# Optimization experiments

Measured on AMD Instinct MI355X. Metric: run time of the kernel, lower is better.

## Reference

```python
import jax, jax.numpy as jnp
import numpy as np

D_EMB = 1024
B, T = 8, 2048

def setup_inputs() -> dict:
    key = jax.random.key(0)
    ks = jax.random.split(key, 7)
    s = 0.02
    return {
        "x": jax.random.normal(ks[0], (B, T, D_EMB), dtype=jnp.float32),
        "W_attn": jax.random.normal(ks[1], (3 * D_EMB, D_EMB), dtype=jnp.float32) * s,
        "b_attn": jax.random.normal(ks[2], (3 * D_EMB,), dtype=jnp.float32) * s,
        "W_proj": jax.random.normal(ks[3], (D_EMB, D_EMB), dtype=jnp.float32) * s,
        "b_proj": jax.random.normal(ks[4], (D_EMB,), dtype=jnp.float32) * s,
        "W_fc": jax.random.normal(ks[5], (1, D_EMB), dtype=jnp.float32) * s,
        "b_fc": jax.random.normal(ks[6], (1,), dtype=jnp.float32) * s,
    }

def reference(x, W_attn, b_attn, W_proj, b_proj, W_fc, b_fc):
    # qkv projection: torch Linear => x @ W.T + b
    qkv = jnp.einsum('btc,dc->btd', x, W_attn) + b_attn          # [B,T,3C]
    q, k, v = jnp.split(qkv, 3, axis=2)                          # each [B,T,C]
    scale = q.shape[-1] ** (-0.5)
    attn_scores = jnp.einsum('btc,bsc->bts', q, k) * scale       # [B,T,T]
    attn_weights = jax.nn.softmax(attn_scores, axis=-1)          # traditional softmax
    y = jnp.einsum('bts,bsc->btc', attn_weights, v)              # [B,T,C]
    y = jnp.einsum('btc,dc->btd', y, W_proj) + b_proj            # [B,T,C]
    out = jnp.einsum('btc,oc->bto', y, W_fc) + b_fc              # [B,T,1]
    return out
```

## Files before the change

### kernel.cpp

```cpp
#include <hip/hip_runtime.h>
#include <stdint.h>

#define D_EMB 1024
#define NBATCH 8
#define SEQ 2048
#define MTOT (NBATCH*SEQ)

typedef __attribute__((ext_vector_type(8))) short short8;
typedef __attribute__((ext_vector_type(4))) float f32x4;

__device__ __forceinline__ ushort bf16r(float x) {
  union { float f; uint32_t u; } c; c.f = x;
  return (ushort)((c.u + 0x7fffu + ((c.u >> 16) & 1u)) >> 16);
}

__device__ __forceinline__ void cp16(const ushort* g, ushort* l) {
  __builtin_amdgcn_global_load_lds(
      (const __attribute__((address_space(1))) void*)g,
      (__attribute__((address_space(3))) void*)l, 16, 0, 0);
}

__global__ __launch_bounds__(256) void cvt_w(
    const float4* __restrict__ Wattn4, const float* __restrict__ bproj,
    const float* __restrict__ Wfc, const float* __restrict__ bfc,
    ushort* __restrict__ wt, float* __restrict__ w_eff, float* __restrict__ wv_eff,
    float* __restrict__ v_eff, float4* __restrict__ numden4, float* __restrict__ sc) {
  int tid = threadIdx.x;
  int b = blockIdx.x;
  __shared__ ushort lt[64][68];
  __shared__ float red[4];
  if (b < 512) {
    int td = b & 31, tc = b >> 5;
    #pragma unroll
    for (int rep = 0; rep < 4; rep++) {
      int i = (tid >> 4) + rep * 16;
      int jj = tid & 15;
      float4 v = Wattn4[(long)(td * 64 + i) * 256 + tc * 16 + jj];
      lt[i][jj * 4 + 0] = bf16r(v.x);
      lt[i][jj * 4 + 1] = bf16r(v.y);
      lt[i][jj * 4 + 2] = bf16r(v.z);
      lt[i][jj * 4 + 3] = bf16r(v.w);
    }
    __syncthreads();
    #pragma unroll
    for (int rep = 0; rep < 2; rep++) {
      int c = (tid >> 3) + rep * 32;
      int d0 = (tid & 7) * 8;
      short8 o;
      #pragma unroll
      for (int k = 0; k < 8; k++) o[k] = (short)lt[d0 + k][c];
      *(short8*)(wt + (long)(tc * 64 + c) * 2048 + td * 64 + d0) = o;
    }
    return;
  }
  int b2 = b - 512;
  if (b2 == 0) {
    for (int i = tid; i < 1024; i += 256) { w_eff[i] = 0.f; wv_eff[i] = 0.f; v_eff[i] = 0.f; }
    return;
  }
  if (b2 == 1) {
    float v = 0.f;
    #pragma unroll
    for (int i = 0; i < 4; i++) { int c = tid + i * 256; v += bproj[c] * Wfc[c]; }
    int lane = tid & 63, w = tid >> 6;
    #pragma unroll
    for (int off = 32; off; off >>= 1) v += __shfl_xor(v, off);
    if (lane == 0) red[w] = v;
    __syncthreads();
    if (tid == 0) sc[0] = red[0] + red[1] + red[2] + red[3] + bfc[0];
    return;
  }
  numden4[(long)(b2 - 2) * 256 + tid] = make_float4(0.f, 0.f, 0.f, 0.f);
}

__global__ void prep1(const float* __restrict__ Wp, const float* __restrict__ Wfc,
                      const float* __restrict__ Wattn, const float* __restrict__ battn,
                      float* __restrict__ w_eff, float* __restrict__ v_eff) {
  int c = blockIdx.x * 256 + threadIdx.x;
  if (blockIdx.y < 64) {
    int d0 = blockIdx.y * 16;
    float s = 0.f;
    #pragma unroll
    for (int d = d0; d < d0 + 16; d++) s += Wfc[d] * Wp[(long)d * D_EMB + c];
    atomicAdd(&w_eff[c], s);
  } else {
    int d0 = (blockIdx.y - 64) * 16;
    float s = 0.f;
    #pragma unroll
    for (int d = d0; d < d0 + 16; d++) s += battn[d] * Wattn[(long)(1024 + d) * D_EMB + c];
    atomicAdd(&v_eff[c], s);
  }
}

__global__ void prep2(const float* __restrict__ Wattn, const float* __restrict__ battn,
                      const float* __restrict__ w_eff, float* __restrict__ wv_eff,
                      float* __restrict__ sc) {
  int tid = threadIdx.x;
  if (blockIdx.y == 64) {
    if (blockIdx.x != 0) return;
    float v = 0.f;
    #pragma unroll
    for (int i = 0; i < 4; i++) { int c = tid + i * 256; v += battn[2048 + c] * w_eff[c]; }
    int lane = tid & 63, w = tid >> 6;
    #pragma unroll
    for (int off = 32; off; off >>= 1) v += __shfl_xor(v, off);
    __shared__ float red[4];
    if (lane == 0) red[w] = v;
    __syncthreads();
    if (tid == 0) sc[1] = red[0] + red[1] + red[2] + red[3];
    return;
  }
  int d = blockIdx.x * 256 + tid;
  int c0 = blockIdx.y * 16;
  float s = 0.f;
  #pragma unroll
  for (int c = c0; c < c0 + 16; c++) s += w_eff[c] * Wattn[(long)(2048 + c) * D_EMB + d];
  atomicAdd(&wv_eff[d], s);
}

template<int MODE>
__device__ __forceinline__ void gemm_body(
    int bx, int by, int z, ushort* lds_a, ushort* lds_b,
    const ushort* __restrict__ A, long lda, long sAz,
    const ushort* __restrict__ B, long ldb, long sBz,
    ushort* __restrict__ C, long ldc, float scale, int K,
    const float* __restrict__ vw, const float* __restrict__ bb,
    float* __restrict__ num, float* __restrict__ den) {
  const ushort* Az = A + (long)z * sAz;
  const ushort* Bz = B + (long)z * sBz;
  long m0 = (long)by * 128, n0 = (long)bx * 128;
  int t = threadIdx.x;
  int wave = t >> 6, lane = t & 63;
  int r = lane & 15, q = lane >> 4;
  int wm = (wave & 1) * 64, wn = (wave >> 1) * 64;

  f32x4 acc[4][4] = {};

  int row0 = t >> 3;
  int kc = (t & 7) ^ (row0 & 7);
  const ushort* Ap = Az + (m0 + row0) * lda + kc * 8;
  const ushort* Bp = Bz + (n0 + row0) * ldb + kc * 8;
  long a32 = 32 * lda, b32 = 32 * ldb;

  int swz = r & 7;

  #pragma unroll 1
  for (int k0 = 0; k0 < K; k0 += 64) {
    if (k0) __syncthreads();
    cp16(Ap + k0,            lds_a + t * 8);
    cp16(Ap + k0 + a32,      lds_a + (t + 256) * 8);
    cp16(Ap + k0 + 2 * a32,  lds_a + (t + 512) * 8);
    cp16(Ap + k0 + 3 * a32,  lds_a + (t + 768) * 8);
    cp16(Bp + k0,            lds_b + t * 8);
    cp16(Bp + k0 + b32,      lds_b + (t + 256) * 8);
    cp16(Bp + k0 + 2 * b32,  lds_b + (t + 512) * 8);
    cp16(Bp + k0 + 3 * b32,  lds_b + (t + 768) * 8);
    __syncthreads();
    #pragma unroll
    for (int kk = 0; kk < 2; kk++) {
      int cidx = (kk * 4 + q) ^ swz;
      short8 af[4], bf[4];
      #pragma unroll
      for (int i = 0; i < 4; i++)
        af[i] = *(const short8*)(lds_a + ((wm + i * 16 + r) * 8 + cidx) * 8);
      #pragma unroll
      for (int j = 0; j < 4; j++)
        bf[j] = *(const short8*)(lds_b + ((wn + j * 16 + r) * 8 + cidx) * 8);
      #pragma unroll
      for (int i = 0; i < 4; i++)
        #pragma unroll
        for (int j = 0; j < 4; j++)
          acc[i][j] = __builtin_amdgcn_mfma_f32_16x16x32_bf16(af[i], bf[j], acc[i][j], 0, 0, 0);
    }
  }

  if (MODE == 0) {
    #pragma unroll
    for (int i = 0; i < 4; i++) {
      #pragma unroll
      for (int j = 0; j < 4; j++) {
        long col = n0 + wn + j * 16 + r;
        #pragma unroll
        for (int rr = 0; rr < 4; rr++) {
          long row = m0 + wm + i * 16 + q * 4 + rr;
          C[row * ldc + col] = bf16r(acc[i][j][rr] * scale);
        }
      }
    }
  } else {
    const float* vwz = vw + (long)z * SEQ + n0;
    const float* bbz = bb + (long)z * SEQ + n0;
    float* numz = num + (long)z * SEQ + m0;
    float* denz = den + (long)z * SEQ + m0;
    float vwj[4], bbj[4];
    #pragma unroll
    for (int j = 0; j < 4; j++) {
      vwj[j] = vwz[wn + j * 16 + r];
      bbj[j] = bbz[wn + j * 16 + r];
    }
    #pragma unroll
    for (int i = 0; i < 4; i++) {
      #pragma unroll
      for (int rr = 0; rr < 4; rr++) {
        float sn = 0.f, sd = 0.f;
        #pragma unroll
        for (int j = 0; j < 4; j++) {
          float e = __expf((acc[i][j][rr] + bbj[j]) * scale);
          sd += e;
          sn += e * vwj[j];
        }
        #pragma unroll
        for (int off = 1; off < 16; off <<= 1) {
          sn += __shfl_xor(sn, off);
          sd += __shfl_xor(sd, off);
        }
        if (r == 0) {
          int row = wm + i * 16 + q * 4 + rr;
          atomicAdd(&numz[row], sn);
          atomicAdd(&denz[row], sd);
        }
      }
    }
  }
}

__global__ __launch_bounds__(256, 4) void cvt_mt(
    const float4* __restrict__ x4, const float4* __restrict__ wv4,
    const float4* __restrict__ v4, const float* __restrict__ sc,
    ushort* __restrict__ xb, float* __restrict__ vw, float* __restrict__ bb,
    const ushort* __restrict__ wt, ushort* __restrict__ mt) {
  __shared__ __align__(16) ushort lds_a[128 * 64];
  __shared__ __align__(16) ushort lds_b[128 * 64];
  int tid = threadIdx.x;
  if (blockIdx.x < 64) {
    int b = blockIdx.x;
    gemm_body<0>(b & 7, b >> 3, 0, lds_a, lds_b,
                 wt + 1024, 2048L, 0L, wt, 2048L, 0L,
                 mt, 1024L, 1.0f, D_EMB, nullptr, nullptr, nullptr, nullptr);
    return;
  }
  int wave = tid >> 6, lane = tid & 63;
  long row = (long)(blockIdx.x - 64) * 4 + wave;
  const float4* xr = x4 + row * 256;
  ushort* xo = xb + row * D_EMB;
  float s = 0.f, s2 = 0.f;
  #pragma unroll
  for (int i = 0; i < 4; i++) {
    int idx = lane + i * 64;
    float4 v = xr[idx];
    float4 w = wv4[idx];
    float4 u = v4[idx];
    *(ushort4*)(xo + idx * 4) = make_ushort4(bf16r(v.x), bf16r(v.y), bf16r(v.z), bf16r(v.w));
    s  += v.x * w.x + v.y * w.y + v.z * w.z + v.w * w.w;
    s2 += v.x * u.x + v.y * u.y + v.z * u.z + v.w * u.w;
  }
  #pragma unroll
  for (int off = 32; off; off >>= 1) { s += __shfl_xor(s, off); s2 += __shfl_xor(s2, off); }
  if (lane == 0) { vw[row] = s + sc[1]; bb[row] = s2; }
}

template<int MODE, int RMODE>
__global__ __launch_bounds__(256, 4) void gemm_nt(
    const ushort* __restrict__ A, long lda, long sAz,
    const ushort* __restrict__ B, long ldb, long sBz,
    ushort* __restrict__ C, long ldc, float scale, int K,
    const float* __restrict__ vw, const float* __restrict__ bb,
    float* __restrict__ num, float* __restrict__ den) {
  __shared__ __align__(16) ushort lds_a[128 * 64];
  __shared__ __align__(16) ushort lds_b[128 * 64];
  int bx, by, z;
  if (RMODE == 1) {
    int f = (int)(blockIdx.x + 8u * blockIdx.y);
    int xcd = f & 7, g = f >> 3;
    by = xcd * 16 + (g & 15); bx = g >> 4; z = 0;
  } else {
    bx = blockIdx.x; by = blockIdx.y; z = blockIdx.z;
  }
  gemm_body<MODE>(bx, by, z, lds_a, lds_b, A, lda, sAz, B, ldb, sBz,
                  C, ldc, scale, K, vw, bb, num, den);
}

__global__ __launch_bounds__(256) void finalize(
    const float* __restrict__ num, const float* __restrict__ den,
    const float* __restrict__ sc, float* __restrict__ out) {
  long i = blockIdx.x * 256L + threadIdx.x;
  out[i] = num[i] / den[i] + sc[0];
}

extern "C" void kernel_launch(void* const* d_in, const int* in_sizes, int n_in,
                              void* d_out, int out_size, void* d_ws, size_t ws_size,
                              hipStream_t stream) {
  const float* x     = (const float*)d_in[0];
  const float* Wattn = (const float*)d_in[1];
  const float* battn = (const float*)d_in[2];
  const float* Wproj = (const float*)d_in[3];
  const float* bproj = (const float*)d_in[4];
  const float* Wfc   = (const float*)d_in[5];
  const float* bfc   = (const float*)d_in[6];
  float* out = (float*)d_out;

  const size_t OFF_XB    = 0;
  const size_t OFF_WT    = 33554432;
  const size_t OFF_MT    = 37748736;
  const size_t OFF_XM    = 39845888;
  const size_t OFF_NUM   = 73400320;
  const size_t OFF_DEN   = 73465856;
  const size_t OFF_VW    = 73531392;
  const size_t OFF_BB    = 73596928;
  const size_t OFF_WEFF  = 73662464;
  const size_t OFF_WVEFF = 73666560;
  const size_t OFF_VEFF  = 73670656;
  const size_t OFF_SC    = 73674752;
  const size_t NEED      = 73674760;
  if (ws_size < NEED) return;

  char* ws = (char*)d_ws;
  ushort* xb    = (ushort*)(ws + OFF_XB);
  ushort* wt    = (ushort*)(ws + OFF_WT);
  ushort* mt    = (ushort*)(ws + OFF_MT);
  ushort* xm    = (ushort*)(ws + OFF_XM);
  float* num    = (float*)(ws + OFF_NUM);
  float* den    = (float*)(ws + OFF_DEN);
  float* vw     = (float*)(ws + OFF_VW);
  float* bb     = (float*)(ws + OFF_BB);
  float* w_eff  = (float*)(ws + OFF_WEFF);
  float* wv_eff = (float*)(ws + OFF_WVEFF);
  float* v_eff  = (float*)(ws + OFF_VEFF);
  float* sc     = (float*)(ws + OFF_SC);

  cvt_w<<<dim3(546), dim3(256), 0, stream>>>(
      (const float4*)Wattn, bproj, Wfc, bfc, wt, w_eff, wv_eff, v_eff, (float4*)num, sc);

  prep1<<<dim3(4, 128), dim3(256), 0, stream>>>(Wproj, Wfc, Wattn, battn, w_eff, v_eff);

  prep2<<<dim3(4, 65), dim3(256), 0, stream>>>(Wattn, battn, w_eff, wv_eff, sc);

  cvt_mt<<<dim3(64 + 4096), dim3(256), 0, stream>>>(
      (const float4*)x, (const float4*)wv_eff, (const float4*)v_eff, sc, xb, vw, bb, wt, mt);

  gemm_nt<0, 1><<<dim3(8, 128, 1), dim3(256), 0, stream>>>(
      xb, (long)D_EMB, 0L, mt, (long)D_EMB, 0L,
      xm, (long)D_EMB, 1.0f, D_EMB, nullptr, nullptr, nullptr, nullptr);

  gemm_nt<1, 0><<<dim3(16, 16, NBATCH), dim3(256), 0, stream>>>(
      xm, (long)D_EMB, (long)SEQ * D_EMB, xb, (long)D_EMB, (long)SEQ * D_EMB,
      nullptr, 0L, 0.03125f, D_EMB, vw, bb, num, den);

  finalize<<<dim3(64), dim3(256), 0, stream>>>(num, den, sc, out);
}
```

Measured before the change: 260.8 us.

## Split-K the Wq·Wk product and fold it into the prep kernels

The 1024x1024 Wq^T·Wk weight product was computed by only 64 blocks with the full K=1024, sharing a launch with the x conversion. It is now split into 8 K-slices of 128. That gives 512 GEMM blocks, which run alongside the prep1 reductions in one launch and write fp32 partials. A new prep2red kernel sums the partials and converts them to bf16, and the x conversion becomes its own kernel. Launch bounds on the GEMM are raised to 5 waves per SIMD. The split adds an fp32 partial buffer round trip through memory in exchange for much more parallelism on the tail-bound weight GEMM.

Result: slower. 555.1 us (+112.9%).

```diff
diff --git a/kernel.cpp b/kernel.cpp
--- a/kernel.cpp
+++ b/kernel.cpp
@@ -73,57 +73,12 @@
   numden4[(long)(b2 - 2) * 256 + tid] = make_float4(0.f, 0.f, 0.f, 0.f);
 }
 
-__global__ void prep1(const float* __restrict__ Wp, const float* __restrict__ Wfc,
-                      const float* __restrict__ Wattn, const float* __restrict__ battn,
-                      float* __restrict__ w_eff, float* __restrict__ v_eff) {
-  int c = blockIdx.x * 256 + threadIdx.x;
-  if (blockIdx.y < 64) {
-    int d0 = blockIdx.y * 16;
-    float s = 0.f;
-    #pragma unroll
-    for (int d = d0; d < d0 + 16; d++) s += Wfc[d] * Wp[(long)d * D_EMB + c];
-    atomicAdd(&w_eff[c], s);
-  } else {
-    int d0 = (blockIdx.y - 64) * 16;
-    float s = 0.f;
-    #pragma unroll
-    for (int d = d0; d < d0 + 16; d++) s += battn[d] * Wattn[(long)(1024 + d) * D_EMB + c];
-    atomicAdd(&v_eff[c], s);
-  }
-}
-
-__global__ void prep2(const float* __restrict__ Wattn, const float* __restrict__ battn,
-                      const float* __restrict__ w_eff, float* __restrict__ wv_eff,
-                      float* __restrict__ sc) {
-  int tid = threadIdx.x;
-  if (blockIdx.y == 64) {
-    if (blockIdx.x != 0) return;
-    float v = 0.f;
-    #pragma unroll
-    for (int i = 0; i < 4; i++) { int c = tid + i * 256; v += battn[2048 + c] * w_eff[c]; }
-    int lane = tid & 63, w = tid >> 6;
-    #pragma unroll
-    for (int off = 32; off; off >>= 1) v += __shfl_xor(v, off);
-    __shared__ float red[4];
-    if (lane == 0) red[w] = v;
-    __syncthreads();
-    if (tid == 0) sc[1] = red[0] + red[1] + red[2] + red[3];
-    return;
-  }
-  int d = blockIdx.x * 256 + tid;
-  int c0 = blockIdx.y * 16;
-  float s = 0.f;
-  #pragma unroll
-  for (int c = c0; c < c0 + 16; c++) s += w_eff[c] * Wattn[(long)(2048 + c) * D_EMB + d];
-  atomicAdd(&wv_eff[d], s);
-}
-
 template<int MODE>
 __device__ __forceinline__ void gemm_body(
     int bx, int by, int z, ushort* lds_a, ushort* lds_b,
     const ushort* __restrict__ A, long lda, long sAz,
     const ushort* __restrict__ B, long ldb, long sBz,
-    ushort* __restrict__ C, long ldc, float scale, int K,
+    ushort* __restrict__ C, long ldc, float* __restrict__ fC, float scale, int K,
     const float* __restrict__ vw, const float* __restrict__ bb,
     float* __restrict__ num, float* __restrict__ den) {
   const ushort* Az = A + (long)z * sAz;
@@ -187,6 +142,20 @@
         }
       }
     }
+  } else if (MODE == 2) {
+    float* fz = fC + (long)z * 1048576;
+    #pragma unroll
+    for (int i = 0; i < 4; i++) {
+      #pragma unroll
+      for (int j = 0; j < 4; j++) {
+        long col = n0 + wn + j * 16 + r;
+        #pragma unroll
+        for (int rr = 0; rr < 4; rr++) {
+          long row = m0 + wm + i * 16 + q * 4 + rr;
+          fz[row * 1024 + col] = acc[i][j][rr];
+        }
+      }
+    }
   } else {
     const float* vwz = vw + (long)z * SEQ + n0;
     const float* bbz = bb + (long)z * SEQ + n0;
@@ -224,23 +193,89 @@
   }
 }
 
-__global__ __launch_bounds__(256, 4) void cvt_mt(
+__global__ __launch_bounds__(256, 5) void prep1mt(
+    const float* __restrict__ Wp, const float* __restrict__ Wfc,
+    const float* __restrict__ Wattn, const float* __restrict__ battn,
+    float* __restrict__ w_eff, float* __restrict__ v_eff,
+    const ushort* __restrict__ wt, float* __restrict__ mtf) {
+  __shared__ __align__(16) ushort lds_a[128 * 64];
+  __shared__ __align__(16) ushort lds_b[128 * 64];
+  int b = blockIdx.x;
+  if (b < 512) {
+    int c = (b & 3) * 256 + threadIdx.x;
+    int y = b >> 2;
+    if (y < 64) {
+      int d0 = y * 16;
+      float s = 0.f;
+      #pragma unroll
+      for (int d = d0; d < d0 + 16; d++) s += Wfc[d] * Wp[(long)d * D_EMB + c];
+      atomicAdd(&w_eff[c], s);
+    } else {
+      int d0 = (y - 64) * 16;
+      float s = 0.f;
+      #pragma unroll
+      for (int d = d0; d < d0 + 16; d++) s += battn[d] * Wattn[(long)(1024 + d) * D_EMB + c];
+      atomicAdd(&v_eff[c], s);
+    }
+    return;
+  }
+  int m = b - 512;
+  int kz = m >> 6, g = m & 63;
+  gemm_body<2>(g & 7, g >> 3, kz, lds_a, lds_b,
+               wt + 1024, 2048L, 128L, wt, 2048L, 128L,
+               nullptr, 0L, mtf, 1.0f, 128, nullptr, nullptr, nullptr, nullptr);
+}
+
+__global__ __launch_bounds__(256) void prep2red(
+    const float* __restrict__ Wattn, const float* __restrict__ battn,
+    const float* __restrict__ w_eff, float* __restrict__ wv_eff,
+    float* __restrict__ sc, const float4* __restrict__ mtf4, ushort* __restrict__ mt) {
+  int tid = threadIdx.x;
+  int y = blockIdx.y;
+  if (y < 64) {
+    int d = blockIdx.x * 256 + tid;
+    int c0 = y * 16;
+    float s = 0.f;
+    #pragma unroll
+    for (int c = c0; c < c0 + 16; c++) s += w_eff[c] * Wattn[(long)(2048 + c) * D_EMB + d];
+    atomicAdd(&wv_eff[d], s);
+    return;
+  }
+  if (y == 64) {
+    if (blockIdx.x != 0) return;
+    float v = 0.f;
+    #pragma unroll
+    for (int i = 0; i < 4; i++) { int c = tid + i * 256; v += battn[2048 + c] * w_eff[c]; }
+    int lane = tid & 63, w = tid >> 6;
+    #pragma unroll
+    for (int off = 32; off; off >>= 1) v += __shfl_xor(v, off);
+    __shared__ float red[4];
+    if (lane == 0) red[w] = v;
+    __syncthreads();
+    if (tid == 0) sc[1] = red[0] + red[1] + red[2] + red[3];
+    return;
+  }
+  int seg = (y - 65) * 4 + blockIdx.x;
+  #pragma unroll
+  for (int jj = 0; jj < 4; jj++) {
+    long p4 = (long)seg * 1024 + tid + 256 * jj;
+    float4 s = mtf4[p4];
+    #pragma unroll
+    for (int kz = 1; kz < 8; kz++) {
+      float4 t2 = mtf4[(long)kz * 262144 + p4];
+      s.x += t2.x; s.y += t2.y; s.z += t2.z; s.w += t2.w;
+    }
+    *(ushort4*)(mt + p4 * 4) = make_ushort4(bf16r(s.x), bf16r(s.y), bf16r(s.z), bf16r(s.w));
+  }
+}
+
+__global__ __launch_bounds__(256) void cvt_x(
     const float4* __restrict__ x4, const float4* __restrict__ wv4,
     const float4* __restrict__ v4, const float* __restrict__ sc,
-    ushort* __restrict__ xb, float* __restrict__ vw, float* __restrict__ bb,
-    const ushort* __restrict__ wt, ushort* __restrict__ mt) {
-  __shared__ __align__(16) ushort lds_a[128 * 64];
-  __shared__ __align__(16) ushort lds_b[128 * 64];
+    ushort* __restrict__ xb, float* __restrict__ vw, float* __restrict__ bb) {
   int tid = threadIdx.x;
-  if (blockIdx.x < 64) {
-    int b = blockIdx.x;
-    gemm_body<0>(b & 7, b >> 3, 0, lds_a, lds_b,
-                 wt + 1024, 2048L, 0L, wt, 2048L, 0L,
-                 mt, 1024L, 1.0f, D_EMB, nullptr, nullptr, nullptr, nullptr);
-    return;
-  }
   int wave = tid >> 6, lane = tid & 63;
-  long row = (long)(blockIdx.x - 64) * 4 + wave;
+  long row = (long)blockIdx.x * 4 + wave;
   const float4* xr = x4 + row * 256;
   ushort* xo = xb + row * D_EMB;
   float s = 0.f, s2 = 0.f;
@@ -260,7 +295,7 @@
 }
 
 template<int MODE, int RMODE>
-__global__ __launch_bounds__(256, 4) void gemm_nt(
+__global__ __launch_bounds__(256, 5) void gemm_nt(
     const ushort* __restrict__ A, long lda, long sAz,
     const ushort* __restrict__ B, long ldb, long sBz,
     ushort* __restrict__ C, long ldc, float scale, int K,
@@ -277,7 +312,7 @@
     bx = blockIdx.x; by = blockIdx.y; z = blockIdx.z;
   }
   gemm_body<MODE>(bx, by, z, lds_a, lds_b, A, lda, sAz, B, ldb, sBz,
-                  C, ldc, scale, K, vw, bb, num, den);
+                  C, ldc, nullptr, scale, K, vw, bb, num, den);
 }
 
 __global__ __launch_bounds__(256) void finalize(
@@ -303,6 +338,7 @@
   const size_t OFF_WT    = 33554432;
   const size_t OFF_MT    = 37748736;
   const size_t OFF_XM    = 39845888;
+  const size_t OFF_MTF   = OFF_XM;
   const size_t OFF_NUM   = 73400320;
   const size_t OFF_DEN   = 73465856;
   const size_t OFF_VW    = 73531392;
@@ -319,6 +355,7 @@
   ushort* wt    = (ushort*)(ws + OFF_WT);
   ushort* mt    = (ushort*)(ws + OFF_MT);
   ushort* xm    = (ushort*)(ws + OFF_XM);
+  float* mtf    = (float*)(ws + OFF_MTF);
   float* num    = (float*)(ws + OFF_NUM);
   float* den    = (float*)(ws + OFF_DEN);
   float* vw     = (float*)(ws + OFF_VW);
@@ -331,12 +368,14 @@
   cvt_w<<<dim3(546), dim3(256), 0, stream>>>(
       (const float4*)Wattn, bproj, Wfc, bfc, wt, w_eff, wv_eff, v_eff, (float4*)num, sc);
 
-  prep1<<<dim3(4, 128), dim3(256), 0, stream>>>(Wproj, Wfc, Wattn, battn, w_eff, v_eff);
-
-  prep2<<<dim3(4, 65), dim3(256), 0, stream>>>(Wattn, battn, w_eff, wv_eff, sc);
-
-  cvt_mt<<<dim3(64 + 4096), dim3(256), 0, stream>>>(
-      (const float4*)x, (const float4*)wv_eff, (const float4*)v_eff, sc, xb, vw, bb, wt, mt);
+  prep1mt<<<dim3(1024), dim3(256), 0, stream>>>(
+      Wproj, Wfc, Wattn, battn, w_eff, v_eff, wt, mtf);
+
+  prep2red<<<dim3(4, 129), dim3(256), 0, stream>>>(
+      Wattn, battn, w_eff, wv_eff, sc, (const float4*)mtf, mt);
+
+  cvt_x<<<dim3(4096), dim3(256), 0, stream>>>(
+      (const float4*)x, (const float4*)wv_eff, (const float4*)v_eff, sc, xb, vw, bb);
 
   gemm_nt<0, 1><<<dim3(8, 128, 1), dim3(256), 0, stream>>>(
       xb, (long)D_EMB, 0L, mt, (long)D_EMB, 0L,
```

## Fuse prep stages into fewer launches and finalize inside the attention GEMM

Applied to the files above, without the earlier changes.

Collapses seven launches into four. The x conversion, weight transpose and partial prep products now run in one kernel, with partial sums written to buffers instead of atomics. The Wq^T Wk GEMM runs alongside the reductions, and the row dot-products run alongside the first big GEMM. The separate finalize pass is removed: the last block per row tile, found through an atomic counter, computes the outputs. This cuts launch gaps and idle tails, at the cost of an extra fence and counter, plus partial-sum buffers that get re-reduced by several blocks.

After: 525.8 us. 2.02x slower.

```diff
diff --git a/kernel.cpp b/kernel.cpp
--- a/kernel.cpp
+++ b/kernel.cpp
@@ -18,104 +18,6 @@
   __builtin_amdgcn_global_load_lds(
       (const __attribute__((address_space(1))) void*)g,
       (__attribute__((address_space(3))) void*)l, 16, 0, 0);
-}
-
-__global__ __launch_bounds__(256) void cvt_w(
-    const float4* __restrict__ Wattn4, const float* __restrict__ bproj,
-    const float* __restrict__ Wfc, const float* __restrict__ bfc,
-    ushort* __restrict__ wt, float* __restrict__ w_eff, float* __restrict__ wv_eff,
-    float* __restrict__ v_eff, float4* __restrict__ numden4, float* __restrict__ sc) {
-  int tid = threadIdx.x;
-  int b = blockIdx.x;
-  __shared__ ushort lt[64][68];
-  __shared__ float red[4];
-  if (b < 512) {
-    int td = b & 31, tc = b >> 5;
-    #pragma unroll
-    for (int rep = 0; rep < 4; rep++) {
-      int i = (tid >> 4) + rep * 16;
-      int jj = tid & 15;
-      float4 v = Wattn4[(long)(td * 64 + i) * 256 + tc * 16 + jj];
-      lt[i][jj * 4 + 0] = bf16r(v.x);
-      lt[i][jj * 4 + 1] = bf16r(v.y);
-      lt[i][jj * 4 + 2] = bf16r(v.z);
-      lt[i][jj * 4 + 3] = bf16r(v.w);
-    }
-    __syncthreads();
-    #pragma unroll
-    for (int rep = 0; rep < 2; rep++) {
-      int c = (tid >> 3) + rep * 32;
-      int d0 = (tid & 7) * 8;
-      short8 o;
-      #pragma unroll
-      for (int k = 0; k < 8; k++) o[k] = (short)lt[d0 + k][c];
-      *(short8*)(wt + (long)(tc * 64 + c) * 2048 + td * 64 + d0) = o;
-    }
-    return;
-  }
-  int b2 = b - 512;
-  if (b2 == 0) {
-    for (int i = tid; i < 1024; i += 256) { w_eff[i] = 0.f; wv_eff[i] = 0.f; v_eff[i] = 0.f; }
-    return;
-  }
-  if (b2 == 1) {
-    float v = 0.f;
-    #pragma unroll
-    for (int i = 0; i < 4; i++) { int c = tid + i * 256; v += bproj[c] * Wfc[c]; }
-    int lane = tid & 63, w = tid >> 6;
-    #pragma unroll
-    for (int off = 32; off; off >>= 1) v += __shfl_xor(v, off);
-    if (lane == 0) red[w] = v;
-    __syncthreads();
-    if (tid == 0) sc[0] = red[0] + red[1] + red[2] + red[3] + bfc[0];
-    return;
-  }
-  numden4[(long)(b2 - 2) * 256 + tid] = make_float4(0.f, 0.f, 0.f, 0.f);
-}
-
-__global__ void prep1(const float* __restrict__ Wp, const float* __restrict__ Wfc,
-                      const float* __restrict__ Wattn, const float* __restrict__ battn,
-                      float* __restrict__ w_eff, float* __restrict__ v_eff) {
-  int c = blockIdx.x * 256 + threadIdx.x;
-  if (blockIdx.y < 64) {
-    int d0 = blockIdx.y * 16;
-    float s = 0.f;
-    #pragma unroll
-    for (int d = d0; d < d0 + 16; d++) s += Wfc[d] * Wp[(long)d * D_EMB + c];
-    atomicAdd(&w_eff[c], s);
-  } else {
-    int d0 = (blockIdx.y - 64) * 16;
-    float s = 0.f;
-    #pragma unroll
-    for (int d = d0; d < d0 + 16; d++) s += battn[d] * Wattn[(long)(1024 + d) * D_EMB + c];
-    atomicAdd(&v_eff[c], s);
-  }
-}
-
-__global__ void prep2(const float* __restrict__ Wattn, const float* __restrict__ battn,
-                      const float* __restrict__ w_eff, float* __restrict__ wv_eff,
-                      float* __restrict__ sc) {
-  int tid = threadIdx.x;
-  if (blockIdx.y == 64) {
-    if (blockIdx.x != 0) return;
-    float v = 0.f;
-    #pragma unroll
-    for (int i = 0; i < 4; i++) { int c = tid + i * 256; v += battn[2048 + c] * w_eff[c]; }
-    int lane = tid & 63, w = tid >> 6;
-    #pragma unroll
-    for (int off = 32; off; off >>= 1) v += __shfl_xor(v, off);
-    __shared__ float red[4];
-    if (lane == 0) red[w] = v;
-    __syncthreads();
-    if (tid == 0) sc[1] = red[0] + red[1] + red[2] + red[3];
-    return;
-  }
-  int d = blockIdx.x * 256 + tid;
-  int c0 = blockIdx.y * 16;
-  float s = 0.f;
-  #pragma unroll
-  for (int c = c0; c < c0 + 16; c++) s += w_eff[c] * Wattn[(long)(2048 + c) * D_EMB + d];
-  atomicAdd(&wv_eff[d], s);
 }
 
 template<int MODE>
@@ -125,7 +27,8 @@
     const ushort* __restrict__ B, long ldb, long sBz,
     ushort* __restrict__ C, long ldc, float scale, int K,
     const float* __restrict__ vw, const float* __restrict__ bb,
-    float* __restrict__ num, float* __restrict__ den) {
+    float* __restrict__ num, float* __restrict__ den,
+    int* __restrict__ cnt, const float* __restrict__ sc, float* __restrict__ out) {
   const ushort* Az = A + (long)z * sAz;
   const ushort* Bz = B + (long)z * sBz;
   long m0 = (long)by * 128, n0 = (long)bx * 128;
@@ -221,28 +124,199 @@
         }
       }
     }
-  }
-}
-
-__global__ __launch_bounds__(256, 4) void cvt_mt(
-    const float4* __restrict__ x4, const float4* __restrict__ wv4,
-    const float4* __restrict__ v4, const float* __restrict__ sc,
-    ushort* __restrict__ xb, float* __restrict__ vw, float* __restrict__ bb,
+    __threadfence();
+    __syncthreads();
+    __shared__ int lastf;
+    if (t == 0) {
+      int old = atomicAdd(&cnt[z * 16 + by], 1);
+      lastf = (old == 15) ? 1 : 0;
+    }
+    __syncthreads();
+    if (lastf) {
+      __threadfence();
+      if (t < 128) {
+        long row = (long)z * SEQ + m0 + t;
+        float nn = atomicAdd(&num[row], 0.f);
+        float dd = atomicAdd(&den[row], 0.f);
+        out[row] = nn / dd + sc[0];
+      }
+    }
+  }
+}
+
+__global__ __launch_bounds__(256) void fuse1(
+    const float4* __restrict__ x4, const float4* __restrict__ Wattn4,
+    const float* __restrict__ Wp, const float* __restrict__ Wfc,
+    const float* __restrict__ Wattn, const float* __restrict__ battn,
+    const float* __restrict__ bproj, const float* __restrict__ bfc,
+    ushort* __restrict__ xb, ushort* __restrict__ wt,
+    float* __restrict__ pw, float* __restrict__ pv,
+    float* __restrict__ wv_eff, float4* __restrict__ numden4,
+    int* __restrict__ cnt, float* __restrict__ sc) {
+  int tid = threadIdx.x;
+  int b = blockIdx.x;
+  __shared__ ushort lt[64][68];
+  __shared__ float red[4];
+  if (b < 4096) {
+    int wave = tid >> 6, lane = tid & 63;
+    long row = (long)b * 4 + wave;
+    const float4* xr = x4 + row * 256;
+    ushort* xo = xb + row * D_EMB;
+    #pragma unroll
+    for (int i = 0; i < 4; i++) {
+      int idx = lane + i * 64;
+      float4 v = xr[idx];
+      *(ushort4*)(xo + idx * 4) = make_ushort4(bf16r(v.x), bf16r(v.y), bf16r(v.z), bf16r(v.w));
+    }
+    return;
+  }
+  if (b < 4608) {
+    int bb_ = b - 4096;
+    int td = bb_ & 31, tc = bb_ >> 5;
+    #pragma unroll
+    for (int rep = 0; rep < 4; rep++) {
+      int i = (tid >> 4) + rep * 16;
+      int jj = tid & 15;
+      float4 v = Wattn4[(long)(td * 64 + i) * 256 + tc * 16 + jj];
+      lt[i][jj * 4 + 0] = bf16r(v.x);
+      lt[i][jj * 4 + 1] = bf16r(v.y);
+      lt[i][jj * 4 + 2] = bf16r(v.z);
+      lt[i][jj * 4 + 3] = bf16r(v.w);
+    }
+    __syncthreads();
+    #pragma unroll
+    for (int rep = 0; rep < 2; rep++) {
+      int c = (tid >> 3) + rep * 32;
+      int d0 = (tid & 7) * 8;
+      short8 o;
+      #pragma unroll
+      for (int k = 0; k < 8; k++) o[k] = (short)lt[d0 + k][c];
+      *(short8*)(wt + (long)(tc * 64 + c) * 2048 + td * 64 + d0) = o;
+    }
+    return;
+  }
+  if (b < 5120) {
+    int m = b - 4608;
+    int c = (m & 3) * 256 + tid;
+    int y = m >> 2;
+    if (y < 64) {
+      int d0 = y * 16;
+      float s = 0.f;
+      #pragma unroll
+      for (int d = d0; d < d0 + 16; d++) s += Wfc[d] * Wp[(long)d * D_EMB + c];
+      pw[(long)y * 1024 + c] = s;
+    } else {
+      int y2 = y - 64;
+      int d0 = y2 * 16;
+      float s = 0.f;
+      #pragma unroll
+      for (int d = d0; d < d0 + 16; d++) s += battn[d] * Wattn[(long)(1024 + d) * D_EMB + c];
+      pv[(long)y2 * 1024 + c] = s;
+    }
+    return;
+  }
+  int b2 = b - 5120;
+  if (b2 == 0) {
+    for (int i = tid; i < 1024; i += 256) wv_eff[i] = 0.f;
+    if (tid < 128) cnt[tid] = 0;
+    return;
+  }
+  if (b2 == 1) {
+    float v = 0.f;
+    #pragma unroll
+    for (int i = 0; i < 4; i++) { int c = tid + i * 256; v += bproj[c] * Wfc[c]; }
+    int lane = tid & 63, w = tid >> 6;
+    #pragma unroll
+    for (int off = 32; off; off >>= 1) v += __shfl_xor(v, off);
+    if (lane == 0) red[w] = v;
+    __syncthreads();
+    if (tid == 0) sc[0] = red[0] + red[1] + red[2] + red[3] + bfc[0];
+    return;
+  }
+  numden4[(long)(b2 - 2) * 256 + tid] = make_float4(0.f, 0.f, 0.f, 0.f);
+}
+
+__global__ __launch_bounds__(256, 4) void fuse2(
+    const float* __restrict__ Wattn, const float* __restrict__ battn,
+    const float* __restrict__ pw, const float* __restrict__ pv,
+    float* __restrict__ wv_eff, float* __restrict__ v_eff, float* __restrict__ sc,
     const ushort* __restrict__ wt, ushort* __restrict__ mt) {
   __shared__ __align__(16) ushort lds_a[128 * 64];
   __shared__ __align__(16) ushort lds_b[128 * 64];
+  __shared__ float redf[16];
   int tid = threadIdx.x;
-  if (blockIdx.x < 64) {
-    int b = blockIdx.x;
-    gemm_body<0>(b & 7, b >> 3, 0, lds_a, lds_b,
-                 wt + 1024, 2048L, 0L, wt, 2048L, 0L,
-                 mt, 1024L, 1.0f, D_EMB, nullptr, nullptr, nullptr, nullptr);
-    return;
-  }
+  int b = blockIdx.x;
+  if (b < 256) {
+    int bx = b & 3, y = b >> 2;
+    int c0 = y * 16;
+    if (tid < 16) {
+      float s = 0.f;
+      #pragma unroll
+      for (int yp = 0; yp < 64; yp++) s += pw[(long)yp * 1024 + c0 + tid];
+      redf[tid] = s;
+    }
+    __syncthreads();
+    int d = bx * 256 + tid;
+    float s = 0.f;
+    #pragma unroll
+    for (int i = 0; i < 16; i++) s += redf[i] * Wattn[(long)(2048 + c0 + i) * D_EMB + d];
+    atomicAdd(&wv_eff[d], s);
+    return;
+  }
+  if (b == 256) {
+    float v = 0.f;
+    #pragma unroll
+    for (int i = 0; i < 4; i++) {
+      int c = tid + i * 256;
+      float wc = 0.f;
+      #pragma unroll
+      for (int yp = 0; yp < 64; yp++) wc += pw[(long)yp * 1024 + c];
+      v += battn[2048 + c] * wc;
+    }
+    int lane = tid & 63, w = tid >> 6;
+    #pragma unroll
+    for (int off = 32; off; off >>= 1) v += __shfl_xor(v, off);
+    if (lane == 0) redf[w] = v;
+    __syncthreads();
+    if (tid == 0) sc[1] = redf[0] + redf[1] + redf[2] + redf[3];
+    return;
+  }
+  if (b < 261) {
+    int c = (b - 257) * 256 + tid;
+    float s = 0.f;
+    #pragma unroll
+    for (int yp = 0; yp < 64; yp++) s += pv[(long)yp * 1024 + c];
+    v_eff[c] = s;
+    return;
+  }
+  int g = b - 261;
+  gemm_body<0>(g & 7, g >> 3, 0, lds_a, lds_b,
+               wt + 1024, 2048L, 0L, wt, 2048L, 0L,
+               mt, 1024L, 1.0f, D_EMB,
+               nullptr, nullptr, nullptr, nullptr, nullptr, nullptr, nullptr);
+}
+
+__global__ __launch_bounds__(256, 4) void gemm1v(
+    const ushort* __restrict__ xb, const ushort* __restrict__ mt, ushort* __restrict__ xm,
+    const float4* __restrict__ x4, const float4* __restrict__ wv4,
+    const float4* __restrict__ v4, const float* __restrict__ sc,
+    float* __restrict__ vw, float* __restrict__ bb) {
+  __shared__ __align__(16) ushort lds_a[128 * 64];
+  __shared__ __align__(16) ushort lds_b[128 * 64];
+  int b = blockIdx.x;
+  if (b < 1024) {
+    int xcd = b & 7, g = b >> 3;
+    int by = xcd * 16 + (g & 15), bx = g >> 4;
+    gemm_body<0>(bx, by, 0, lds_a, lds_b,
+                 xb, (long)D_EMB, 0L, mt, (long)D_EMB, 0L,
+                 xm, (long)D_EMB, 1.0f, D_EMB,
+                 nullptr, nullptr, nullptr, nullptr, nullptr, nullptr, nullptr);
+    return;
+  }
+  int tid = threadIdx.x;
   int wave = tid >> 6, lane = tid & 63;
-  long row = (long)(blockIdx.x - 64) * 4 + wave;
+  long row = (long)(b - 1024) * 4 + wave;
   const float4* xr = x4 + row * 256;
-  ushort* xo = xb + row * D_EMB;
   float s = 0.f, s2 = 0.f;
   #pragma unroll
   for (int i = 0; i < 4; i++) {
@@ -250,7 +324,6 @@
     float4 v = xr[idx];
     float4 w = wv4[idx];
     float4 u = v4[idx];
-    *(ushort4*)(xo + idx * 4) = make_ushort4(bf16r(v.x), bf16r(v.y), bf16r(v.z), bf16r(v.w));
     s  += v.x * w.x + v.y * w.y + v.z * w.z + v.w * w.w;
     s2 += v.x * u.x + v.y * u.y + v.z * u.z + v.w * u.w;
   }
@@ -259,32 +332,16 @@
   if (lane == 0) { vw[row] = s + sc[1]; bb[row] = s2; }
 }
 
-template<int MODE, int RMODE>
-__global__ __launch_bounds__(256, 4) void gemm_nt(
-    const ushort* __restrict__ A, long lda, long sAz,
-    const ushort* __restrict__ B, long ldb, long sBz,
-    ushort* __restrict__ C, long ldc, float scale, int K,
+__global__ __launch_bounds__(256, 4) void gemm2f(
+    const ushort* __restrict__ xm, const ushort* __restrict__ xb,
     const float* __restrict__ vw, const float* __restrict__ bb,
-    float* __restrict__ num, float* __restrict__ den) {
+    float* __restrict__ num, float* __restrict__ den,
+    int* __restrict__ cnt, const float* __restrict__ sc, float* __restrict__ out) {
   __shared__ __align__(16) ushort lds_a[128 * 64];
   __shared__ __align__(16) ushort lds_b[128 * 64];
-  int bx, by, z;
-  if (RMODE == 1) {
-    int f = (int)(blockIdx.x + 8u * blockIdx.y);
-    int xcd = f & 7, g = f >> 3;
-    by = xcd * 16 + (g & 15); bx = g >> 4; z = 0;
-  } else {
-    bx = blockIdx.x; by = blockIdx.y; z = blockIdx.z;
-  }
-  gemm_body<MODE>(bx, by, z, lds_a, lds_b, A, lda, sAz, B, ldb, sBz,
-                  C, ldc, scale, K, vw, bb, num, den);
-}
-
-__global__ __launch_bounds__(256) void finalize(
-    const float* __restrict__ num, const float* __restrict__ den,
-    const float* __restrict__ sc, float* __restrict__ out) {
-  long i = blockIdx.x * 256L + threadIdx.x;
-  out[i] = num[i] / den[i] + sc[0];
+  gemm_body<1>(blockIdx.x, blockIdx.y, blockIdx.z, lds_a, lds_b,
+               xm, (long)D_EMB, (long)SEQ * D_EMB, xb, (long)D_EMB, (long)SEQ * D_EMB,
+               nullptr, 0L, 0.03125f, D_EMB, vw, bb, num, den, cnt, sc, out);
 }
 
 extern "C" void kernel_launch(void* const* d_in, const int* in_sizes, int n_in,
@@ -307,11 +364,13 @@
   const size_t OFF_DEN   = 73465856;
   const size_t OFF_VW    = 73531392;
   const size_t OFF_BB    = 73596928;
-  const size_t OFF_WEFF  = 73662464;
-  const size_t OFF_WVEFF = 73666560;
-  const size_t OFF_VEFF  = 73670656;
-  const size_t OFF_SC    = 73674752;
-  const size_t NEED      = 73674760;
+  const size_t OFF_PW    = 73662464;
+  const size_t OFF_PV    = 73924608;
+  const size_t OFF_WVEFF = 74186752;
+  const size_t OFF_VEFF  = 74190848;
+  const size_t OFF_SC    = 74194944;
+  const size_t OFF_CNT   = 74195008;
+  const size_t NEED      = 74195520;
   if (ws_size < NEED) return;
 
   char* ws = (char*)d_ws;
@@ -323,28 +382,23 @@
   float* den    = (float*)(ws + OFF_DEN);
   float* vw     = (float*)(ws + OFF_VW);
   float* bb     = (float*)(ws + OFF_BB);
-  float* w_eff  = (float*)(ws + OFF_WEFF);
+  float* pw     = (float*)(ws + OFF_PW);
+  float* pv     = (float*)(ws + OFF_PV);
   float* wv_eff = (float*)(ws + OFF_WVEFF);
   float* v_eff  = (float*)(ws + OFF_VEFF);
   float* sc     = (float*)(ws + OFF_SC);
-
-  cvt_w<<<dim3(546), dim3(256), 0, stream>>>(
-      (const float4*)Wattn, bproj, Wfc, bfc, wt, w_eff, wv_eff, v_eff, (float4*)num, sc);
-
-  prep1<<<dim3(4, 128), dim3(256), 0, stream>>>(Wproj, Wfc, Wattn, battn, w_eff, v_eff);
-
-  prep2<<<dim3(4, 65), dim3(256), 0, stream>>>(Wattn, battn, w_eff, wv_eff, sc);
-
-  cvt_mt<<<dim3(64 + 4096), dim3(256), 0, stream>>>(
-      (const float4*)x, (const float4*)wv_eff, (const float4*)v_eff, sc, xb, vw, bb, wt, mt);
-
-  gemm_nt<0, 1><<<dim3(8, 128, 1), dim3(256), 0, stream>>>(
-      xb, (long)D_EMB, 0L, mt, (long)D_EMB, 0L,
-      xm, (long)D_EMB, 1.0f, D_EMB, nullptr, nullptr, nullptr, nullptr);
-
-  gemm_nt<1, 0><<<dim3(16, 16, NBATCH), dim3(256), 0, stream>>>(
-      xm, (long)D_EMB, (long)SEQ * D_EMB, xb, (long)D_EMB, (long)SEQ * D_EMB,
-      nullptr, 0L, 0.03125f, D_EMB, vw, bb, num, den);
-
-  finalize<<<dim3(64), dim3(256), 0, stream>>>(num, den, sc, out);
-}
+  int*   cnt    = (int*)(ws + OFF_CNT);
+
+  fuse1<<<dim3(5154), dim3(256), 0, stream>>>(
+      (const float4*)x, (const float4*)Wattn, Wproj, Wfc, Wattn, battn, bproj, bfc,
+      xb, wt, pw, pv, wv_eff, (float4*)num, cnt, sc);
+
+  fuse2<<<dim3(325), dim3(256), 0, stream>>>(
+      Wattn, battn, pw, pv, wv_eff, v_eff, sc, wt, mt);
+
+  gemm1v<<<dim3(5120), dim3(256), 0, stream>>>(
+      xb, mt, xm, (const float4*)x, (const float4*)wv_eff, (const float4*)v_eff, sc, vw, bb);
+
+  gemm2f<<<dim3(16, 16, NBATCH), dim3(256), 0, stream>>>(
+      xm, xb, vw, bb, num, den, cnt, sc, out);
+}
```
